# Performance work log

Measured on AMD Instinct MI355X. Metric: run time of the kernel, lower is better.

## Reference

```python
import jax, jax.numpy as jnp
import numpy as np

B, S, DM = 4, 8192, 1024
N_RED = 16384   # tokens merged into their right neighbor
N_SAVE = 16384  # tokens kept; must be divisible by B


def setup_inputs() -> dict:
    key = jax.random.key(0)
    k1, k2, k3, k4 = jax.random.split(key, 4)
    x = jax.random.normal(k1, (B, S, DM), dtype=jnp.float32)
    W = jax.random.normal(k2, (DM, DM), dtype=jnp.float32) * (1.0 / np.sqrt(DM))
    ids_to_reduce = jax.random.randint(k3, (N_RED,), 0, B * S - 1, dtype=jnp.int64)
    ids_to_save = jax.random.randint(k4, (N_SAVE,), 0, B * S, dtype=jnp.int64)
    return {"x": x, "W": W, "ids_to_save": ids_to_save, "ids_to_reduce": ids_to_reduce}


def reference(x, W, ids_to_save, ids_to_reduce):
    batch_size, _, dm = x.shape
    xf = x.reshape(-1, dm)                       # [B*S, dm]
    reduced = xf[ids_to_reduce]                  # gather  [N_RED, dm]
    transformed = (reduced @ W.T).astype(jnp.float32)  # Linear, no bias
    xf = xf.at[ids_to_reduce + 1].add(transformed)     # scatter-add into right neighbor
    saved = xf[ids_to_save]                      # gather  [N_SAVE, dm]
    return saved.reshape(batch_size, -1, dm)     # [B, N_SAVE//B, dm]
```

## Files before the change

### kernel.cpp

```cpp
#include <hip/hip_runtime.h>

#define DM    1024
#define NTOK  32768
#define NRED  16384
#define NSAVE 16384
#define MMAX  16384

typedef __attribute__((ext_vector_type(8)))  short bf16x8;
typedef __attribute__((ext_vector_type(4)))  float f32x4;
typedef __attribute__((ext_vector_type(16))) float f32x16;

__device__ __forceinline__ ushort f2bf(float f) {
    union { float f; unsigned u; } v; v.f = f;
    unsigned r = (v.u + 0x7FFF + ((v.u >> 16) & 1)) >> 16;
    return (ushort)r;
}
__device__ __forceinline__ float bf2f(ushort u) {
    union { unsigned u; float f; } v; v.u = ((unsigned)u) << 16;
    return v.f;
}

__global__ __launch_bounds__(256) void setup_kernel(const float* __restrict__ W,
                                                    ushort* __restrict__ Wb,
                                                    int* __restrict__ cnt,
                                                    int* __restrict__ need,
                                                    int* __restrict__ counter) {
    int t = blockIdx.x * 256 + threadIdx.x;
    float4 v = ((const float4*)W)[t];
    ushort4 o;
    o.x = f2bf(v.x); o.y = f2bf(v.y); o.z = f2bf(v.z); o.w = f2bf(v.w);
    ((ushort4*)Wb)[t] = o;
    if (t < NTOK) { cnt[t] = 0; need[t] = 0; }
    if (t == 0) *counter = 0;
}

__global__ __launch_bounds__(256) void prep_kernel(const int* __restrict__ red,
                                                   const int* __restrict__ sav,
                                                   int* __restrict__ cnt,
                                                   int* __restrict__ need) {
    int j = blockIdx.x * 256 + threadIdx.x;
    if (j >= NRED) return;
    atomicAdd(&cnt[red[j]], 1);
    int s = sav[j];
    if (s > 0) need[s - 1] = 1;
}

__global__ __launch_bounds__(256) void compact_kernel(const int* __restrict__ cnt,
                                                      const int* __restrict__ need,
                                                      int* __restrict__ inv,
                                                      int* __restrict__ list,
                                                      int* __restrict__ counter) {
    int t = blockIdx.x * 256 + threadIdx.x;
    if (t >= NTOK) return;
    if (need[t] && cnt[t] > 0) {
        int pos = atomicAdd(counter, 1);
        inv[t] = pos;
        list[pos] = t;
    }
}

__global__ __launch_bounds__(256) void convx_kernel(const float* __restrict__ X,
                                                    const int* __restrict__ list,
                                                    const int* __restrict__ counter,
                                                    ushort* __restrict__ Xb) {
    const int M = *counter;
    const int Mpad = (M + 127) & ~127;
    for (int r = blockIdx.x; r < Mpad; r += gridDim.x) {
        ushort4 o;
        if (r < M) {
            int src = list[r];
            float4 v = ((const float4*)(X + (size_t)src * DM))[threadIdx.x];
            o.x = f2bf(v.x); o.y = f2bf(v.y); o.z = f2bf(v.z); o.w = f2bf(v.w);
        } else {
            o.x = 0; o.y = 0; o.z = 0; o.w = 0;
        }
        ((ushort4*)(Xb + (size_t)r * DM))[threadIdx.x] = o;
    }
}

__global__ __launch_bounds__(128) void gemm_kernel(const ushort* __restrict__ Xb,
                                                   const ushort* __restrict__ Wb,
                                                   const int* __restrict__ counter,
                                                   ushort* __restrict__ Tb) {
    const int M = *counter;
    const int m0 = blockIdx.x * 128;
    if (m0 >= M) return;
    const int n0 = blockIdx.y * 128;

    __shared__ char lds[65536];

    const int tid = threadIdx.x;
    const int l   = tid & 63;
    const int w   = tid >> 6;

    const int srow   = l >> 3;
    const int schunk = (l & 7) ^ (srow & 7);
    const ushort* aS = Xb + (size_t)(m0 + w * 64 + srow) * DM + schunk * 8;
    const ushort* bS = Wb + (size_t)(n0 + w * 64 + srow) * DM + schunk * 8;

#define STAGE(buf, k0) do {                                                          \
    char* _d = lds + (buf) * 32768 + w * 8192;                                       \
    _Pragma("unroll")                                                                \
    for (int _i = 0; _i < 8; ++_i) {                                                 \
        __builtin_amdgcn_global_load_lds(                                            \
            (const __attribute__((address_space(1))) unsigned*)(aS + (k0) + _i * 8 * DM), \
            (__attribute__((address_space(3))) unsigned*)(_d + _i * 1024), 16, 0, 0);      \
        __builtin_amdgcn_global_load_lds(                                            \
            (const __attribute__((address_space(1))) unsigned*)(bS + (k0) + _i * 8 * DM), \
            (__attribute__((address_space(3))) unsigned*)(_d + 16384 + _i * 1024), 16, 0, 0); \
    }                                                                                \
} while (0)

    const int h  = l >> 5;
    const int e  = l & 7;
    const int r32 = l & 31;
    int arow[2], brow[4];
#pragma unroll
    for (int fm = 0; fm < 2; ++fm) arow[fm] = (w * 64 + fm * 32 + r32) * 128;
#pragma unroll
    for (int fn = 0; fn < 4; ++fn) brow[fn] = 16384 + (fn * 32 + r32) * 128;

    f32x16 acc[2][4] = {};

    STAGE(0, 0);
#pragma unroll
    for (int t = 0; t < 16; ++t) {
        const char* base = lds + (t & 1) * 32768;
        if (t < 15) {
            STAGE((t & 1) ^ 1, (t + 1) * 64);
            asm volatile("s_waitcnt vmcnt(16)" ::: "memory");
        } else {
            asm volatile("s_waitcnt vmcnt(0)" ::: "memory");
        }
        __builtin_amdgcn_sched_barrier(0);
        __builtin_amdgcn_s_barrier();

#pragma unroll
        for (int ks = 0; ks < 4; ++ks) {
            const int cs = (((ks * 2 + h) ^ e) << 4);
            bf16x8 af[2], bfr[4];
#pragma unroll
            for (int fm = 0; fm < 2; ++fm) af[fm]  = *(const bf16x8*)(base + arow[fm] + cs);
#pragma unroll
            for (int fn = 0; fn < 4; ++fn) bfr[fn] = *(const bf16x8*)(base + brow[fn] + cs);
#pragma unroll
            for (int fm = 0; fm < 2; ++fm)
#pragma unroll
                for (int fn = 0; fn < 4; ++fn)
                    acc[fm][fn] = __builtin_amdgcn_mfma_f32_32x32x16_bf16(af[fm], bfr[fn], acc[fm][fn], 0, 0, 0);
        }

        if (t < 15)
            __builtin_amdgcn_s_barrier();
    }
#undef STAGE

#pragma unroll
    for (int fm = 0; fm < 2; ++fm) {
        int mband = m0 + w * 64 + fm * 32;
#pragma unroll
        for (int fn = 0; fn < 4; ++fn) {
            int n = n0 + fn * 32 + r32;
#pragma unroll
            for (int r = 0; r < 16; ++r) {
                int m = mband + (r & 3) + 8 * (r >> 2) + 4 * h;
                if (m < M) Tb[(size_t)m * DM + n] = f2bf(acc[fm][fn][r]);
            }
        }
    }
}

__global__ __launch_bounds__(256) void out_kernel(const float* __restrict__ X,
                                                  const ushort* __restrict__ Tb,
                                                  const int* __restrict__ sav,
                                                  const int* __restrict__ cnt,
                                                  const int* __restrict__ inv,
                                                  float* __restrict__ out) {
    int r = blockIdx.x;
    int d = threadIdx.x;
    int s = sav[r];
    const float4* xr = (const float4*)(X + (size_t)s * DM);
    float4 v = xr[d];
    if (s > 0) {
        int t = s - 1;
        int c = cnt[t];
        if (c > 0) {
            float fc = (float)c;
            const ushort4* tr = (const ushort4*)(Tb + (size_t)inv[t] * DM);
            ushort4 wv = tr[d];
            v.x += fc * bf2f(wv.x); v.y += fc * bf2f(wv.y);
            v.z += fc * bf2f(wv.z); v.w += fc * bf2f(wv.w);
        }
    }
    ((float4*)out)[(size_t)r * (DM / 4) + d] = v;
}

extern "C" void kernel_launch(void* const* d_in, const int* in_sizes, int n_in,
                              void* d_out, int out_size, void* d_ws, size_t ws_size,
                              hipStream_t stream) {
    const float* X   = (const float*)d_in[0];
    const float* W   = (const float*)d_in[1];
    const int*   sav = (const int*)d_in[2];
    const int*   red = (const int*)d_in[3];
    float* out = (float*)d_out;

    char* ws = (char*)d_ws;
    int* counter = (int*)ws;
    int* cnt  = counter + 64;
    int* need = cnt + NTOK;
    int* inv  = need + NTOK;
    int* list = inv + NTOK;
    ushort* Wb = (ushort*)(ws + (1 << 19));
    ushort* Xb = (ushort*)(ws + (4 << 20));
    ushort* Tb = (ushort*)(ws + (36u << 20));

    setup_kernel<<<DM * DM / 4 / 256, 256, 0, stream>>>(W, Wb, cnt, need, counter);
    prep_kernel<<<NRED / 256, 256, 0, stream>>>(red, sav, cnt, need);
    compact_kernel<<<NTOK / 256, 256, 0, stream>>>(cnt, need, inv, list, counter);
    convx_kernel<<<2048, 256, 0, stream>>>(X, list, counter, Xb);

    dim3 ggrid(MMAX / 128, DM / 128);
    gemm_kernel<<<ggrid, 128, 0, stream>>>(Xb, Wb, counter, Tb);

    out_kernel<<<NSAVE, 256, 0, stream>>>(X, Tb, sav, cnt, inv, out);
}
```

Measured before the change: 69.63 us.

## Split GEMM K dimension in two and use 4-wave 2x2 warp tiling

The GEMM grid gains a z dimension that splits the K=1024 reduction into two halves, each writing a bf16 partial result to its own buffer. Blocks grow from 2 to 4 waves arranged 2x2, so each wave holds a 64x64 accumulator instead of 64x128. The output kernel reads and sums both partials. The aim is more blocks and waves in flight per CU to improve latency hiding. The cost is twice the partial-result write and read traffic, plus an extra bf16 rounding of each half before summation.

```diff
diff --git a/kernel.cpp b/kernel.cpp
--- a/kernel.cpp
+++ b/kernel.cpp
@@ -1,10 +1,12 @@
 #include <hip/hip_runtime.h>
 
-#define DM    1024
-#define NTOK  32768
-#define NRED  16384
-#define NSAVE 16384
-#define MMAX  16384
+#define DM     1024
+#define NTOK   32768
+#define NRED   16384
+#define NSAVE  16384
+#define MMAX   16384
+#define SPLITK 2
+#define KWIN   (DM / SPLITK)
 
 typedef __attribute__((ext_vector_type(8)))  short bf16x8;
 typedef __attribute__((ext_vector_type(4)))  float f32x4;
@@ -78,14 +80,16 @@
     }
 }
 
-__global__ __launch_bounds__(128) void gemm_kernel(const ushort* __restrict__ Xb,
+__global__ __launch_bounds__(256) void gemm_kernel(const ushort* __restrict__ Xb,
                                                    const ushort* __restrict__ Wb,
                                                    const int* __restrict__ counter,
-                                                   ushort* __restrict__ Tb) {
+                                                   ushort* __restrict__ Tp) {
     const int M = *counter;
     const int m0 = blockIdx.x * 128;
     if (m0 >= M) return;
     const int n0 = blockIdx.y * 128;
+    const int kbase = blockIdx.z * KWIN;
+    ushort* Tout = Tp + (size_t)blockIdx.z * MMAX * DM;
 
     __shared__ char lds[65536];
 
@@ -95,40 +99,42 @@
 
     const int srow   = l >> 3;
     const int schunk = (l & 7) ^ (srow & 7);
-    const ushort* aS = Xb + (size_t)(m0 + w * 64 + srow) * DM + schunk * 8;
-    const ushort* bS = Wb + (size_t)(n0 + w * 64 + srow) * DM + schunk * 8;
+    const ushort* aS = Xb + (size_t)(m0 + w * 32 + srow) * DM + kbase + schunk * 8;
+    const ushort* bS = Wb + (size_t)(n0 + w * 32 + srow) * DM + kbase + schunk * 8;
+    const int dOff = w * 4096;
 
 #define STAGE(buf, k0) do {                                                          \
-    char* _d = lds + (buf) * 32768 + w * 8192;                                       \
+    char* _a = lds + (buf) * 32768 + dOff;                                           \
     _Pragma("unroll")                                                                \
-    for (int _i = 0; _i < 8; ++_i) {                                                 \
+    for (int _i = 0; _i < 4; ++_i) {                                                 \
         __builtin_amdgcn_global_load_lds(                                            \
             (const __attribute__((address_space(1))) unsigned*)(aS + (k0) + _i * 8 * DM), \
-            (__attribute__((address_space(3))) unsigned*)(_d + _i * 1024), 16, 0, 0);      \
+            (__attribute__((address_space(3))) unsigned*)(_a + _i * 1024), 16, 0, 0);      \
         __builtin_amdgcn_global_load_lds(                                            \
             (const __attribute__((address_space(1))) unsigned*)(bS + (k0) + _i * 8 * DM), \
-            (__attribute__((address_space(3))) unsigned*)(_d + 16384 + _i * 1024), 16, 0, 0); \
+            (__attribute__((address_space(3))) unsigned*)(_a + 16384 + _i * 1024), 16, 0, 0); \
     }                                                                                \
 } while (0)
 
-    const int h  = l >> 5;
-    const int e  = l & 7;
+    const int wm  = w >> 1, wn = w & 1;
+    const int h   = l >> 5;
+    const int e   = l & 7;
     const int r32 = l & 31;
-    int arow[2], brow[4];
-#pragma unroll
-    for (int fm = 0; fm < 2; ++fm) arow[fm] = (w * 64 + fm * 32 + r32) * 128;
-#pragma unroll
-    for (int fn = 0; fn < 4; ++fn) brow[fn] = 16384 + (fn * 32 + r32) * 128;
-
-    f32x16 acc[2][4] = {};
+    int arow[2], brow[2];
+#pragma unroll
+    for (int fm = 0; fm < 2; ++fm) arow[fm] = (wm * 64 + fm * 32 + r32) * 128;
+#pragma unroll
+    for (int fn = 0; fn < 2; ++fn) brow[fn] = 16384 + (wn * 64 + fn * 32 + r32) * 128;
+
+    f32x16 acc[2][2] = {};
 
     STAGE(0, 0);
 #pragma unroll
-    for (int t = 0; t < 16; ++t) {
+    for (int t = 0; t < 8; ++t) {
         const char* base = lds + (t & 1) * 32768;
-        if (t < 15) {
+        if (t < 7) {
             STAGE((t & 1) ^ 1, (t + 1) * 64);
-            asm volatile("s_waitcnt vmcnt(16)" ::: "memory");
+            asm volatile("s_waitcnt vmcnt(8)" ::: "memory");
         } else {
             asm volatile("s_waitcnt vmcnt(0)" ::: "memory");
         }
@@ -138,40 +144,40 @@
 #pragma unroll
         for (int ks = 0; ks < 4; ++ks) {
             const int cs = (((ks * 2 + h) ^ e) << 4);
-            bf16x8 af[2], bfr[4];
+            bf16x8 af[2], bfr[2];
 #pragma unroll
             for (int fm = 0; fm < 2; ++fm) af[fm]  = *(const bf16x8*)(base + arow[fm] + cs);
 #pragma unroll
-            for (int fn = 0; fn < 4; ++fn) bfr[fn] = *(const bf16x8*)(base + brow[fn] + cs);
+            for (int fn = 0; fn < 2; ++fn) bfr[fn] = *(const bf16x8*)(base + brow[fn] + cs);
 #pragma unroll
             for (int fm = 0; fm < 2; ++fm)
 #pragma unroll
-                for (int fn = 0; fn < 4; ++fn)
+                for (int fn = 0; fn < 2; ++fn)
                     acc[fm][fn] = __builtin_amdgcn_mfma_f32_32x32x16_bf16(af[fm], bfr[fn], acc[fm][fn], 0, 0, 0);
         }
 
-        if (t < 15)
+        if (t < 7)
             __builtin_amdgcn_s_barrier();
     }
 #undef STAGE
 
 #pragma unroll
     for (int fm = 0; fm < 2; ++fm) {
-        int mband = m0 + w * 64 + fm * 32;
-#pragma unroll
-        for (int fn = 0; fn < 4; ++fn) {
-            int n = n0 + fn * 32 + r32;
+        int mband = m0 + wm * 64 + fm * 32;
+#pragma unroll
+        for (int fn = 0; fn < 2; ++fn) {
+            int n = n0 + wn * 64 + fn * 32 + r32;
 #pragma unroll
             for (int r = 0; r < 16; ++r) {
                 int m = mband + (r & 3) + 8 * (r >> 2) + 4 * h;
-                if (m < M) Tb[(size_t)m * DM + n] = f2bf(acc[fm][fn][r]);
+                if (m < M) Tout[(size_t)m * DM + n] = f2bf(acc[fm][fn][r]);
             }
         }
     }
 }
 
 __global__ __launch_bounds__(256) void out_kernel(const float* __restrict__ X,
-                                                  const ushort* __restrict__ Tb,
+                                                  const ushort* __restrict__ Tp,
                                                   const int* __restrict__ sav,
                                                   const int* __restrict__ cnt,
                                                   const int* __restrict__ inv,
@@ -186,10 +192,13 @@
         int c = cnt[t];
         if (c > 0) {
             float fc = (float)c;
-            const ushort4* tr = (const ushort4*)(Tb + (size_t)inv[t] * DM);
-            ushort4 wv = tr[d];
-            v.x += fc * bf2f(wv.x); v.y += fc * bf2f(wv.y);
-            v.z += fc * bf2f(wv.z); v.w += fc * bf2f(wv.w);
+            size_t rowoff = (size_t)inv[t] * DM;
+            ushort4 p0 = ((const ushort4*)(Tp + rowoff))[d];
+            ushort4 p1 = ((const ushort4*)(Tp + (size_t)MMAX * DM + rowoff))[d];
+            v.x += fc * (bf2f(p0.x) + bf2f(p1.x));
+            v.y += fc * (bf2f(p0.y) + bf2f(p1.y));
+            v.z += fc * (bf2f(p0.z) + bf2f(p1.z));
+            v.w += fc * (bf2f(p0.w) + bf2f(p1.w));
         }
     }
     ((float4*)out)[(size_t)r * (DM / 4) + d] = v;
@@ -212,15 +221,15 @@
     int* list = inv + NTOK;
     ushort* Wb = (ushort*)(ws + (1 << 19));
     ushort* Xb = (ushort*)(ws + (4 << 20));
-    ushort* Tb = (ushort*)(ws + (36u << 20));
+    ushort* Tp = (ushort*)(ws + (36u << 20));
 
     setup_kernel<<<DM * DM / 4 / 256, 256, 0, stream>>>(W, Wb, cnt, need, counter);
     prep_kernel<<<NRED / 256, 256, 0, stream>>>(red, sav, cnt, need);
     compact_kernel<<<NTOK / 256, 256, 0, stream>>>(cnt, need, inv, list, counter);
     convx_kernel<<<2048, 256, 0, stream>>>(X, list, counter, Xb);
 
-    dim3 ggrid(MMAX / 128, DM / 128);
-    gemm_kernel<<<ggrid, 128, 0, stream>>>(Xb, Wb, counter, Tb);
-
-    out_kernel<<<NSAVE, 256, 0, stream>>>(X, Tb, sav, cnt, inv, out);
-}
+    dim3 ggrid(MMAX / 128, DM / 128, SPLITK);
+    gemm_kernel<<<ggrid, 256, 0, stream>>>(Xb, Wb, counter, Tp);
+
+    out_kernel<<<NSAVE, 256, 0, stream>>>(X, Tp, sav, cnt, inv, out);
+}
```

After: 73.91 us. 6.1% more time.
